# Optimization experiments

Hardware: AMD Instinct MI355X
Metric: run time of the kernel (lower is better)

Reference implementation:

```python
import jax, jax.numpy as jnp
import numpy as np

N_NODES = 100000
N_EDGES = 1600000
IN_F = 16
OUT_F = 64
PERIODS = 12
N_PHASE = 4


def setup_inputs() -> dict:
    key = jax.random.key(0)
    ks = jax.random.split(key, 12)
    inp = {
        'x': jax.random.normal(ks[0], (N_NODES, IN_F, PERIODS), jnp.float32),
        'edge_index': jax.random.randint(ks[1], (2, N_EDGES), 0, N_NODES, jnp.int64),
        'attn': jax.random.normal(ks[2], (PERIODS,), jnp.float32),
        'conv_z_w': jax.random.normal(ks[3], (IN_F, OUT_F), jnp.float32) * 0.1,
        'conv_z_b': jnp.zeros((OUT_F,), jnp.float32),
        'conv_r_w': jax.random.normal(ks[4], (IN_F, OUT_F), jnp.float32) * 0.1,
        'conv_r_b': jnp.zeros((OUT_F,), jnp.float32),
        'conv_h_w': jax.random.normal(ks[5], (IN_F, OUT_F), jnp.float32) * 0.1,
        'conv_h_b': jnp.zeros((OUT_F,), jnp.float32),
        'lin_z_w': jax.random.normal(ks[6], (2 * OUT_F, OUT_F), jnp.float32) * 0.1,
        'lin_z_b': jnp.zeros((OUT_F,), jnp.float32),
        'lin_r_w': jax.random.normal(ks[7], (2 * OUT_F, OUT_F), jnp.float32) * 0.1,
        'lin_r_b': jnp.zeros((OUT_F,), jnp.float32),
        'lin_h_w': jax.random.normal(ks[8], (2 * OUT_F, OUT_F), jnp.float32) * 0.1,
        'lin_h_b': jnp.zeros((OUT_F,), jnp.float32),
        'out_w': jax.random.normal(ks[9], (OUT_F, N_PHASE), jnp.float32) * 0.1,
        'out_b': jnp.zeros((N_PHASE,), jnp.float32),
    }
    return inp


def _gcn_norm(edge_index, num_nodes, dtype):
    # add self loops (fill value 1), symmetric normalization as in PyG gcn_norm
    loops = jnp.arange(num_nodes, dtype=edge_index.dtype)
    src = jnp.concatenate([edge_index[0], loops])
    dst = jnp.concatenate([edge_index[1], loops])
    deg = jax.ops.segment_sum(jnp.ones_like(dst, dtype=dtype), dst, num_segments=num_nodes)
    dinv = jnp.where(deg > 0, jax.lax.rsqrt(deg), jnp.zeros_like(deg))
    norm = dinv[src] * dinv[dst]  # [E + N]
    return src, dst, norm


def reference(x, edge_index, attn, conv_z_w, conv_z_b, conv_r_w, conv_r_b,
              conv_h_w, conv_h_b, lin_z_w, lin_z_b, lin_r_w, lin_r_b,
              lin_h_w, lin_h_b, out_w, out_b):
    N = x.shape[0]
    periods = x.shape[2]
    F_out = conv_z_w.shape[1]
    src, dst, norm = _gcn_norm(edge_index, N, x.dtype)

    def conv(Xp, W, b):
        XW = Xp @ W                                   # [N, F_out]
        msg = norm[:, None] * XW[src]                 # gather over edges
        return jax.ops.segment_sum(msg, dst, num_segments=N) + b

    probs = jax.nn.softmax(attn)
    H0 = jnp.zeros((N, F_out), x.dtype)  # A3TGCN never carries H between periods
    H_accum = jnp.zeros((N, F_out), x.dtype)
    for p in range(periods):
        Xp = x[:, :, p]
        Z = jax.nn.sigmoid(jnp.concatenate([conv(Xp, conv_z_w, conv_z_b), H0], axis=1) @ lin_z_w + lin_z_b)
        R = jax.nn.sigmoid(jnp.concatenate([conv(Xp, conv_r_w, conv_r_b), H0], axis=1) @ lin_r_w + lin_r_b)
        Ht = jnp.tanh(jnp.concatenate([conv(Xp, conv_h_w, conv_h_b), H0 * R], axis=1) @ lin_h_w + lin_h_b)
        H = Z * H0 + (1.0 - Z) * Ht
        H_accum = H_accum + probs[p] * H

    h = jax.nn.relu(H_accum)
    logits = h @ out_w + out_b
    return jax.nn.softmax(logits, axis=1)
```

## Files before the change

### kernel.cpp

```cpp
#include <hip/hip_runtime.h>
#include <math.h>

#define NN 100000
#define NE 1600000
#define PERIODS 12
#define SLOTS 48
#define NBUCK 391
#define FRAG 256
#define CAPB 48
#define PTH 512

typedef unsigned short ushort_t;
typedef __attribute__((ext_vector_type(8))) short short8;
typedef __attribute__((ext_vector_type(16))) float floatx16;
typedef __attribute__((ext_vector_type(2))) float f32x2;

union F4S8 { float4 f; short8 s; int4 i; };

__device__ __forceinline__ ushort_t f2bf(float f) {
  unsigned u = __float_as_uint(f);
  unsigned r = u + 0x7fffu + ((u >> 16) & 1u);
  return (ushort_t)(r >> 16);
}

__device__ __forceinline__ f32x2 unpk(unsigned u) {
  f32x2 t;
  t.x = __uint_as_float(u << 16);
  t.y = __uint_as_float(u & 0xffff0000u);
  return t;
}
__device__ __forceinline__ void pkadd(f32x2& a, f32x2 t) {
  asm("v_pk_add_f32 %0, %0, %1" : "+v"(a) : "v"(t));
}

__global__ __launch_bounds__(PTH) void k_part(
    const int* __restrict__ src, const int* __restrict__ dst,
    int* __restrict__ cnt_blk, int* __restrict__ part,
    const float* __restrict__ attn,
    const float* __restrict__ czw, const float* __restrict__ czb,
    const float* __restrict__ chw, const float* __restrict__ chb,
    const float* __restrict__ lzw, const float* __restrict__ lzb,
    const float* __restrict__ lhw, const float* __restrict__ lhb,
    ushort_t* __restrict__ Bz32, ushort_t* __restrict__ Bh32,
    float2* __restrict__ cb2, float* __restrict__ probs_ext) {
  if (blockIdx.x == FRAG) {
    for (int t5 = threadIdx.x; t5 < 1024; t5 += PTH) {
      int f = t5 >> 6, c = t5 & 63;
      float az = 0.f, ah = 0.f;
#pragma unroll 8
      for (int k = 0; k < 64; ++k) {
        az += czw[f * 64 + k] * lzw[k * 64 + c];
        ah += chw[f * 64 + k] * lhw[k * 64 + c];
      }
      int idx = (((c >> 5) * 64) + ((f >> 3) * 32) + (c & 31)) * 8 + (f & 7);
      Bz32[idx] = f2bf(az);
      Bh32[idx] = f2bf(ah);
    }
    if (threadIdx.x < 64) {
      int t = threadIdx.x;
      float vz = lzb[t], vh = lhb[t];
      for (int k = 0; k < 64; ++k) {
        vz += czb[k] * lzw[k * 64 + t];
        vh += chb[k] * lhw[k * 64 + t];
      }
      cb2[t] = make_float2(vz, vh);
    }
    if (threadIdx.x == 0) {
      float m = -1e30f;
      for (int p = 0; p < PERIODS; ++p) m = fmaxf(m, attn[p]);
      float e[PERIODS], s = 0.f;
      for (int p = 0; p < PERIODS; ++p) { e[p] = __expf(attn[p] - m); s += e[p]; }
      float inv = 1.f / s;
      for (int r = 0; r < 32; ++r)
        probs_ext[r] = (r < 12) ? e[r] * inv : ((r < 24) ? e[r - 12] * inv : 0.f);
    }
    return;
  }
  __shared__ int cnt[NBUCK];
  int tid = threadIdx.x, blk = blockIdx.x;
  for (int c = tid; c < NBUCK; c += PTH) cnt[c] = 0;
  __syncthreads();
  for (unsigned i = blk * (unsigned)PTH + tid; i < NE / 4; i += FRAG * (unsigned)PTH) {
    int4 dv = ((const int4*)dst)[i];
    int4 sv = ((const int4*)src)[i];
    int d[4] = {dv.x, dv.y, dv.z, dv.w};
    int s[4] = {sv.x, sv.y, sv.z, sv.w};
#pragma unroll
    for (int k = 0; k < 4; ++k) {
      int cls = d[k] >> 8;
      int slot = atomicAdd(&cnt[cls], 1);
      if (slot < CAPB)
        part[(size_t)(cls * FRAG + blk) * CAPB + slot] = (d[k] & 255) | (s[k] << 8);
    }
  }
  __syncthreads();
  for (int c = tid; c < NBUCK; c += PTH) cnt_blk[blk * NBUCK + c] = cnt[c];
}

__global__ __launch_bounds__(512) void k_csr(const int* __restrict__ cnt_blk,
                                             const int* __restrict__ part,
                                             int* __restrict__ deg,
                                             int* __restrict__ csr) {
  __shared__ int cnt[256];
  int b = blockIdx.x, tid = threadIdx.x;
  if (tid < 256) cnt[tid] = 0;
  __syncthreads();
  int f = tid & 255, sub = tid >> 8;
  int c = cnt_blk[f * NBUCK + b];
  c = c < CAPB ? c : CAPB;
  const int* cell = part + (size_t)(b * FRAG + f) * CAPB;
  for (int i = sub; i < c; i += 2) {
    int r = cell[i];
    int dl = r & 255;
    int slot = atomicAdd(&cnt[dl], 1);
    if (slot < SLOTS)
      csr[((size_t)(b * 256 + dl)) * SLOTS + slot] = (r >> 8) * 384;
  }
  __syncthreads();
  int node = b * 256 + tid;
  if (tid < 256 && node < NN) {
    int cc = cnt[tid];
    deg[node] = cc;
    int cl = cc < SLOTS ? cc : SLOTS;
    int padded = (cl + 3) & ~3;
    int* row = csr + (size_t)node * SLOTS;
    for (int sl = cl; sl < padded; ++sl) row[sl] = NN * 384;
  }
}

__global__ __launch_bounds__(256) void k_prescale(const float* __restrict__ x,
                                                  const int* __restrict__ deg,
                                                  ushort_t* __restrict__ xs) {
  __shared__ float st[4][192];
  int wid = threadIdx.x >> 6, l = threadIdx.x & 63;
  int n = blockIdx.x * 4 + wid;
  if (n > NN || l >= 48) return;
  char* ob = (char*)xs;
  if (n == NN) {
    uint2 z; z.x = 0u; z.y = 0u;
    *(uint2*)(ob + (size_t)NN * 384 + l * 8) = z;
    return;
  }
  float4 v4 = *(const float4*)(x + (size_t)n * 192 + 4 * l);
  *(float4*)&st[wid][4 * l] = v4;
  asm volatile("s_waitcnt lgkmcnt(0)" ::: "memory");
  float dn = rsqrtf((float)(deg[n] + 1));
  float v[4];
#pragma unroll
  for (int c = 0; c < 4; ++c) {
    int o = 4 * l + c;
    v[c] = dn * st[wid][(o & 15) * 12 + (o >> 4)];
  }
  uint2 w;
  w.x = (unsigned)f2bf(v[0]) | ((unsigned)f2bf(v[1]) << 16);
  w.y = (unsigned)f2bf(v[2]) | ((unsigned)f2bf(v[3]) << 16);
  *(uint2*)(ob + (size_t)n * 384 + l * 8) = w;
}

__global__ __launch_bounds__(256) void k_main(
    const ushort_t* __restrict__ xs, const int* __restrict__ csr,
    const int* __restrict__ deg,
    const ushort_t* __restrict__ Bz32, const ushort_t* __restrict__ Bh32,
    const float2* __restrict__ cb2, const float* __restrict__ probs_ext,
    const float* __restrict__ out_w, const float* __restrict__ out_b,
    float* __restrict__ out) {
  __shared__ ushort_t Alds[4][32][16];
  int wid = __builtin_amdgcn_readfirstlane(threadIdx.x >> 6);
  int l = threadIdx.x & 63;
  int nA = blockIdx.x * 8 + wid * 2;
  int nB = nA + 1;
  char* albase = (char*)&Alds[wid][0][0];
  if (l < 16) *(int4*)(albase + 768 + l * 16) = make_int4(0, 0, 0, 0);

  const char* xb = (const char*)xs;
  unsigned loff = (unsigned)(l < 48 ? l : 47) * 8u;

  int2 dd = *(const int2*)(deg + nA);
  int dA = dd.x, dB = dd.y;
  int cA = dA < SLOTS ? dA : SLOTS, cB = dB < SLOTS ? dB : SLOTS;
  int KA = (cA + 3) >> 2, KB = (cB + 3) >> 2;
  const int* bktA = csr + (size_t)nA * SLOTS;
  const int* bktB = bktA + SLOTS;

  uint2 sA = *(const uint2*)(xb + (unsigned)nA * 384u + loff);
  uint2 sB = *(const uint2*)(xb + (unsigned)nB * 384u + loff);
  f32x2 aA01 = unpk(sA.x), aA23 = unpk(sA.y);
  f32x2 aB01 = unpk(sB.x), aB23 = unpk(sB.y);

  uint2 qa[4], qb[4];
  auto issue4 = [&](const int* bkt, int k, uint2* q) {
    int4 e = ((const int4*)bkt)[k];
    q[0] = *(const uint2*)(xb + (unsigned)e.x + loff);
    q[1] = *(const uint2*)(xb + (unsigned)e.y + loff);
    q[2] = *(const uint2*)(xb + (unsigned)e.z + loff);
    q[3] = *(const uint2*)(xb + (unsigned)e.w + loff);
  };
  auto accA4 = [&](const uint2* q) {
#pragma unroll
    for (int j = 0; j < 4; ++j) { pkadd(aA01, unpk(q[j].x)); pkadd(aA23, unpk(q[j].y)); }
  };
  auto accB4 = [&](const uint2* q) {
#pragma unroll
    for (int j = 0; j < 4; ++j) { pkadd(aB01, unpk(q[j].x)); pkadd(aB23, unpk(q[j].y)); }
  };

  int km = KA < KB ? KA : KB;
  int k = 0;
  for (; k < km; ++k) {
    issue4(bktA, k, qa);
    issue4(bktB, k, qb);
    accA4(qa);
    accB4(qb);
  }
  for (; k < KA; ++k) { issue4(bktA, k, qa); accA4(qa); }
  for (; k < KB; ++k) { issue4(bktB, k, qb); accB4(qb); }

  float dnA = rsqrtf((float)(dA + 1)), dnB = rsqrtf((float)(dB + 1));

  if (l < 48) {
    uint2 wA, wB;
    wA.x = (unsigned)f2bf(dnA * aA01.x) | ((unsigned)f2bf(dnA * aA01.y) << 16);
    wA.y = (unsigned)f2bf(dnA * aA23.x) | ((unsigned)f2bf(dnA * aA23.y) << 16);
    wB.x = (unsigned)f2bf(dnB * aB01.x) | ((unsigned)f2bf(dnB * aB01.y) << 16);
    wB.y = (unsigned)f2bf(dnB * aB23.x) | ((unsigned)f2bf(dnB * aB23.y) << 16);
    *(uint2*)(albase + l * 8) = wA;
    *(uint2*)(albase + 384 + l * 8) = wB;
  }
  asm volatile("s_waitcnt lgkmcnt(0)" ::: "memory");
  F4S8 afr;
  afr.f = *(const float4*)(albase + (unsigned)(l & 31) * 32u + (unsigned)(l >> 5) * 16u);

  float2 cbv0 = cb2[l & 31], cbv1 = cb2[(l & 31) + 32];
  float prv[12];
  unsigned sby = (l & 32u) >> 1;
#pragma unroll
  for (int r = 0; r < 12; ++r) {
    const int rb = (r & 3) + 8 * (r >> 2);
    prv[r] = *(const float*)((const char*)probs_ext + rb * 4 + sby);
  }
  bool sh = (l & 32) != 0;
  float hA[2], hB[2];

  floatx16 zero16;
#pragma unroll
  for (int r = 0; r < 16; ++r) zero16[r] = 0.f;

  auto gates = [&](const floatx16& az, const floatx16& ah, float2 cbv, int t) {
    float g0 = 0.f, g1 = 0.f, g2 = 0.f;
#pragma unroll
    for (int r = 0; r < 12; ++r) {
      float zz = az[r] + cbv.x;
      float hh = ah[r] + cbv.y;
      float ez = __expf(zz);
      float e2h = __expf(2.f * hh);
      float val = (e2h - 1.f) * __builtin_amdgcn_rcpf((1.f + ez) * (e2h + 1.f));
      float c = prv[r] * val;
      if ((r >> 2) == 0) g0 += c;
      else if ((r >> 2) == 1) g1 += c;
      else g2 += c;
    }
    float pa = g0 + (sh ? 0.f : g1);
    float pb = g2 + (sh ? g1 : 0.f);
    pa += __shfl_xor(pa, 32, 64);
    pb += __shfl_xor(pb, 32, 64);
    hA[t] = fmaxf(pa, 0.f);
    hB[t] = fmaxf(pb, 0.f);
  };

  {
    F4S8 bz, bh;
    bz.f = ((const float4*)Bz32)[l];
    bh.f = ((const float4*)Bh32)[l];
    floatx16 az = __builtin_amdgcn_mfma_f32_32x32x16_bf16(afr.s, bz.s, zero16, 0, 0, 0);
    floatx16 ah = __builtin_amdgcn_mfma_f32_32x32x16_bf16(afr.s, bh.s, zero16, 0, 0, 0);
    gates(az, ah, cbv0, 0);
  }
  __builtin_amdgcn_sched_barrier(0);
  {
    F4S8 bz, bh;
    bz.f = ((const float4*)Bz32)[64 + l];
    bh.f = ((const float4*)Bh32)[64 + l];
    floatx16 az = __builtin_amdgcn_mfma_f32_32x32x16_bf16(afr.s, bz.s, zero16, 0, 0, 0);
    floatx16 ah = __builtin_amdgcn_mfma_f32_32x32x16_bf16(afr.s, bh.s, zero16, 0, 0, 0);
    gates(az, ah, cbv1, 1);
  }

  int c0 = l & 31;
  float4 w0 = ((const float4*)out_w)[c0];
  float4 w1 = ((const float4*)out_w)[c0 + 32];
  float h0 = sh ? hB[0] : hA[0];
  float h1 = sh ? hB[1] : hA[1];
  float l0 = h0 * w0.x; l0 = fmaf(h1, w1.x, l0);
  float l1 = h0 * w0.y; l1 = fmaf(h1, w1.y, l1);
  float l2 = h0 * w0.z; l2 = fmaf(h1, w1.z, l2);
  float l3 = h0 * w0.w; l3 = fmaf(h1, w1.w, l3);
#pragma unroll
  for (int o = 1; o < 32; o <<= 1) {
    l0 += __shfl_xor(l0, o, 64);
    l1 += __shfl_xor(l1, o, 64);
    l2 += __shfl_xor(l2, o, 64);
    l3 += __shfl_xor(l3, o, 64);
  }
  l0 += out_b[0]; l1 += out_b[1]; l2 += out_b[2]; l3 += out_b[3];
  float m = fmaxf(fmaxf(l0, l1), fmaxf(l2, l3));
  float e0 = __expf(l0 - m), e1 = __expf(l1 - m), e2 = __expf(l2 - m), e3 = __expf(l3 - m);
  float inv = __builtin_amdgcn_rcpf(e0 + e1 + e2 + e3);
  if (c0 < 4) {
    float v = (c0 == 0) ? e0 * inv : (c0 == 1) ? e1 * inv : (c0 == 2) ? e2 * inv : e3 * inv;
    out[(size_t)(sh ? nB : nA) * 4 + c0] = v;
  }
}

extern "C" void kernel_launch(void* const* d_in, const int* in_sizes, int n_in,
                              void* d_out, int out_size, void* d_ws, size_t ws_size,
                              hipStream_t stream) {
  const float* x    = (const float*)d_in[0];
  const int*   ei   = (const int*)d_in[1];
  const float* attn = (const float*)d_in[2];
  const float* czw  = (const float*)d_in[3];
  const float* czb  = (const float*)d_in[4];
  const float* chw  = (const float*)d_in[7];
  const float* chb  = (const float*)d_in[8];
  const float* lzw  = (const float*)d_in[9];
  const float* lzb  = (const float*)d_in[10];
  const float* lhw  = (const float*)d_in[13];
  const float* lhb  = (const float*)d_in[14];
  const float* outw = (const float*)d_in[15];
  const float* outb = (const float*)d_in[16];
  float* out = (float*)d_out;

  char* ws = (char*)d_ws;
  size_t off = 0;
  auto alloc = [&](size_t bytes) {
    void* p = ws + off;
    off += (bytes + 255) & ~(size_t)255;
    return p;
  };
  int*      deg       = (int*)alloc((size_t)NN * 4);
  int*      csr       = (int*)alloc((size_t)NN * SLOTS * 4);
  void*     shared_region = alloc((size_t)(NN + 1) * 384);
  int*      part      = (int*)shared_region;
  ushort_t* xs        = (ushort_t*)shared_region;
  int*      cnt_blk   = (int*)alloc((size_t)FRAG * NBUCK * 4);
  ushort_t* Bz32      = (ushort_t*)alloc(2 * 64 * 8 * 2);
  ushort_t* Bh32      = (ushort_t*)alloc(2 * 64 * 8 * 2);
  float2*   cb2       = (float2*)alloc(64 * 8);
  float*    probs_ext = (float*)alloc(32 * 4);

  k_part<<<FRAG + 1, PTH, 0, stream>>>(ei, ei + NE, cnt_blk, part,
                                       attn, czw, czb, chw, chb,
                                       lzw, lzb, lhw, lhb,
                                       Bz32, Bh32, cb2, probs_ext);
  k_csr<<<NBUCK, 512, 0, stream>>>(cnt_blk, part, deg, csr);
  k_prescale<<<NN / 4 + 1, 256, 0, stream>>>(x, deg, xs);
  k_main<<<NN / 8, 256, 0, stream>>>(xs, csr, deg, Bz32, Bh32, cb2, probs_ext,
                                     outw, outb, out);
}
```

Before: 289.1 us.

## Fuse partition, CSR build and prescale into one cooperative kernel

```diff
diff --git a/kernel.cpp b/kernel.cpp
--- a/kernel.cpp
+++ b/kernel.cpp
@@ -1,5 +1,8 @@
 #include <hip/hip_runtime.h>
+#include <hip/hip_cooperative_groups.h>
 #include <math.h>
+
+namespace cg = cooperative_groups;
 
 #define NN 100000
 #define NE 1600000
@@ -8,7 +11,7 @@
 #define NBUCK 391
 #define FRAG 256
 #define CAPB 48
-#define PTH 512
+#define CGRID 1024
 
 typedef unsigned short ushort_t;
 typedef __attribute__((ext_vector_type(8))) short short8;
@@ -33,7 +36,7 @@
   asm("v_pk_add_f32 %0, %0, %1" : "+v"(a) : "v"(t));
 }
 
-__global__ __launch_bounds__(PTH) void k_part(
+__global__ __launch_bounds__(256) void k_prep(
     const int* __restrict__ src, const int* __restrict__ dst,
     int* __restrict__ cnt_blk, int* __restrict__ part,
     const float* __restrict__ attn,
@@ -42,9 +45,17 @@
     const float* __restrict__ lzw, const float* __restrict__ lzb,
     const float* __restrict__ lhw, const float* __restrict__ lhb,
     ushort_t* __restrict__ Bz32, ushort_t* __restrict__ Bh32,
-    float2* __restrict__ cb2, float* __restrict__ probs_ext) {
-  if (blockIdx.x == FRAG) {
-    for (int t5 = threadIdx.x; t5 < 1024; t5 += PTH) {
+    float2* __restrict__ cb2, float* __restrict__ probs_ext,
+    int* __restrict__ deg, int* __restrict__ csr,
+    const float* __restrict__ x, ushort_t* __restrict__ xs) {
+  cg::grid_group grid = cg::this_grid();
+  __shared__ int cntp[NBUCK];
+  __shared__ int cnt2[256];
+  __shared__ float st[4][192];
+  int blk = blockIdx.x, tid = threadIdx.x;
+
+  if (blk == CGRID - 1) {
+    for (int t5 = tid; t5 < 1024; t5 += 256) {
       int f = t5 >> 6, c = t5 & 63;
       float az = 0.f, ah = 0.f;
 #pragma unroll 8
@@ -56,8 +67,8 @@
       Bz32[idx] = f2bf(az);
       Bh32[idx] = f2bf(ah);
     }
-    if (threadIdx.x < 64) {
-      int t = threadIdx.x;
+    if (tid < 64) {
+      int t = tid;
       float vz = lzb[t], vh = lhb[t];
       for (int k = 0; k < 64; ++k) {
         vz += czb[k] * lzw[k * 64 + t];
@@ -65,7 +76,7 @@
       }
       cb2[t] = make_float2(vz, vh);
     }
-    if (threadIdx.x == 0) {
+    if (tid == 0) {
       float m = -1e30f;
       for (int p = 0; p < PERIODS; ++p) m = fmaxf(m, attn[p]);
       float e[PERIODS], s = 0.f;
@@ -74,87 +85,88 @@
       for (int r = 0; r < 32; ++r)
         probs_ext[r] = (r < 12) ? e[r] * inv : ((r < 24) ? e[r - 12] * inv : 0.f);
     }
-    return;
-  }
-  __shared__ int cnt[NBUCK];
-  int tid = threadIdx.x, blk = blockIdx.x;
-  for (int c = tid; c < NBUCK; c += PTH) cnt[c] = 0;
-  __syncthreads();
-  for (unsigned i = blk * (unsigned)PTH + tid; i < NE / 4; i += FRAG * (unsigned)PTH) {
-    int4 dv = ((const int4*)dst)[i];
-    int4 sv = ((const int4*)src)[i];
-    int d[4] = {dv.x, dv.y, dv.z, dv.w};
-    int s[4] = {sv.x, sv.y, sv.z, sv.w};
-#pragma unroll
-    for (int k = 0; k < 4; ++k) {
-      int cls = d[k] >> 8;
-      int slot = atomicAdd(&cnt[cls], 1);
-      if (slot < CAPB)
-        part[(size_t)(cls * FRAG + blk) * CAPB + slot] = (d[k] & 255) | (s[k] << 8);
-    }
-  }
-  __syncthreads();
-  for (int c = tid; c < NBUCK; c += PTH) cnt_blk[blk * NBUCK + c] = cnt[c];
-}
-
-__global__ __launch_bounds__(512) void k_csr(const int* __restrict__ cnt_blk,
-                                             const int* __restrict__ part,
-                                             int* __restrict__ deg,
-                                             int* __restrict__ csr) {
-  __shared__ int cnt[256];
-  int b = blockIdx.x, tid = threadIdx.x;
-  if (tid < 256) cnt[tid] = 0;
-  __syncthreads();
-  int f = tid & 255, sub = tid >> 8;
-  int c = cnt_blk[f * NBUCK + b];
-  c = c < CAPB ? c : CAPB;
-  const int* cell = part + (size_t)(b * FRAG + f) * CAPB;
-  for (int i = sub; i < c; i += 2) {
-    int r = cell[i];
-    int dl = r & 255;
-    int slot = atomicAdd(&cnt[dl], 1);
-    if (slot < SLOTS)
-      csr[((size_t)(b * 256 + dl)) * SLOTS + slot] = (r >> 8) * 384;
-  }
-  __syncthreads();
-  int node = b * 256 + tid;
-  if (tid < 256 && node < NN) {
-    int cc = cnt[tid];
-    deg[node] = cc;
-    int cl = cc < SLOTS ? cc : SLOTS;
-    int padded = (cl + 3) & ~3;
-    int* row = csr + (size_t)node * SLOTS;
-    for (int sl = cl; sl < padded; ++sl) row[sl] = NN * 384;
-  }
-}
-
-__global__ __launch_bounds__(256) void k_prescale(const float* __restrict__ x,
-                                                  const int* __restrict__ deg,
-                                                  ushort_t* __restrict__ xs) {
-  __shared__ float st[4][192];
-  int wid = threadIdx.x >> 6, l = threadIdx.x & 63;
-  int n = blockIdx.x * 4 + wid;
-  if (n > NN || l >= 48) return;
-  char* ob = (char*)xs;
-  if (n == NN) {
-    uint2 z; z.x = 0u; z.y = 0u;
-    *(uint2*)(ob + (size_t)NN * 384 + l * 8) = z;
-    return;
-  }
-  float4 v4 = *(const float4*)(x + (size_t)n * 192 + 4 * l);
-  *(float4*)&st[wid][4 * l] = v4;
-  asm volatile("s_waitcnt lgkmcnt(0)" ::: "memory");
-  float dn = rsqrtf((float)(deg[n] + 1));
-  float v[4];
-#pragma unroll
-  for (int c = 0; c < 4; ++c) {
-    int o = 4 * l + c;
-    v[c] = dn * st[wid][(o & 15) * 12 + (o >> 4)];
-  }
-  uint2 w;
-  w.x = (unsigned)f2bf(v[0]) | ((unsigned)f2bf(v[1]) << 16);
-  w.y = (unsigned)f2bf(v[2]) | ((unsigned)f2bf(v[3]) << 16);
-  *(uint2*)(ob + (size_t)n * 384 + l * 8) = w;
+  } else if (blk < FRAG) {
+    for (int c = tid; c < NBUCK; c += 256) cntp[c] = 0;
+    __syncthreads();
+    for (unsigned i = blk * 256u + tid; i < NE / 4; i += FRAG * 256u) {
+      int4 dv = ((const int4*)dst)[i];
+      int4 sv = ((const int4*)src)[i];
+      int d[4] = {dv.x, dv.y, dv.z, dv.w};
+      int s[4] = {sv.x, sv.y, sv.z, sv.w};
+#pragma unroll
+      for (int k = 0; k < 4; ++k) {
+        int cls = d[k] >> 8;
+        int slot = atomicAdd(&cntp[cls], 1);
+        if (slot < CAPB)
+          part[(size_t)(cls * FRAG + blk) * CAPB + slot] = (d[k] & 255) | (s[k] << 8);
+      }
+    }
+    __syncthreads();
+    for (int c = tid; c < NBUCK; c += 256) cnt_blk[blk * NBUCK + c] = cntp[c];
+  }
+  grid.sync();
+
+  if (blk < NBUCK) {
+    cnt2[tid] = 0;
+    __syncthreads();
+    int b = blk, f = tid;
+    int c = cnt_blk[f * NBUCK + b];
+    c = c < CAPB ? c : CAPB;
+    const int* cell = part + (size_t)(b * FRAG + f) * CAPB;
+    for (int i = 0; i < c; i += 4) {
+      int4 r4 = *(const int4*)(cell + i);
+      int rr[4] = {r4.x, r4.y, r4.z, r4.w};
+#pragma unroll
+      for (int j = 0; j < 4; ++j) {
+        if (i + j < c) {
+          int r = rr[j];
+          int dl = r & 255;
+          int slot = atomicAdd(&cnt2[dl], 1);
+          if (slot < SLOTS)
+            csr[((size_t)(b * 256 + dl)) * SLOTS + slot] = (r >> 8) * 384;
+        }
+      }
+    }
+    __syncthreads();
+    int node = b * 256 + tid;
+    if (node < NN) {
+      int cc = cnt2[tid];
+      deg[node] = cc;
+      int cl = cc < SLOTS ? cc : SLOTS;
+      int padded = (cl + 3) & ~3;
+      int* row = csr + (size_t)node * SLOTS;
+      for (int sl = cl; sl < padded; ++sl) row[sl] = NN * 384;
+    }
+  }
+  grid.sync();
+
+  {
+    int wid = tid >> 6, l = tid & 63;
+    char* ob = (char*)xs;
+    for (int g = blk; g <= NN / 4; g += CGRID) {
+      int n = g * 4 + wid;
+      if (n > NN || l >= 48) continue;
+      if (n == NN) {
+        uint2 z; z.x = 0u; z.y = 0u;
+        *(uint2*)(ob + (size_t)NN * 384 + l * 8) = z;
+        continue;
+      }
+      float4 v4 = *(const float4*)(x + (size_t)n * 192 + 4 * l);
+      *(float4*)&st[wid][4 * l] = v4;
+      asm volatile("s_waitcnt lgkmcnt(0)" ::: "memory");
+      float dn = rsqrtf((float)(deg[n] + 1));
+      float v[4];
+#pragma unroll
+      for (int c = 0; c < 4; ++c) {
+        int o = 4 * l + c;
+        v[c] = dn * st[wid][(o & 15) * 12 + (o >> 4)];
+      }
+      uint2 w;
+      w.x = (unsigned)f2bf(v[0]) | ((unsigned)f2bf(v[1]) << 16);
+      w.y = (unsigned)f2bf(v[2]) | ((unsigned)f2bf(v[3]) << 16);
+      *(uint2*)(ob + (size_t)n * 384 + l * 8) = w;
+    }
+  }
 }
 
 __global__ __launch_bounds__(256) void k_main(
@@ -347,12 +359,17 @@
   float2*   cb2       = (float2*)alloc(64 * 8);
   float*    probs_ext = (float*)alloc(32 * 4);
 
-  k_part<<<FRAG + 1, PTH, 0, stream>>>(ei, ei + NE, cnt_blk, part,
-                                       attn, czw, czb, chw, chb,
-                                       lzw, lzb, lhw, lhb,
-                                       Bz32, Bh32, cb2, probs_ext);
-  k_csr<<<NBUCK, 512, 0, stream>>>(cnt_blk, part, deg, csr);
-  k_prescale<<<NN / 4 + 1, 256, 0, stream>>>(x, deg, xs);
+  const int* srcp = ei;
+  const int* dstp = ei + NE;
+  void* kargs[] = {
+    (void*)&srcp, (void*)&dstp, (void*)&cnt_blk, (void*)&part,
+    (void*)&attn, (void*)&czw, (void*)&czb, (void*)&chw, (void*)&chb,
+    (void*)&lzw, (void*)&lzb, (void*)&lhw, (void*)&lhb,
+    (void*)&Bz32, (void*)&Bh32, (void*)&cb2, (void*)&probs_ext,
+    (void*)&deg, (void*)&csr, (void*)&x, (void*)&xs
+  };
+  hipLaunchCooperativeKernel((const void*)k_prep, dim3(CGRID), dim3(256),
+                             kargs, 0, stream);
   k_main<<<NN / 8, 256, 0, stream>>>(xs, csr, deg, Bz32, Bh32, cb2, probs_ext,
                                      outw, outb, out);
 }
```

Measured after the change: 576.1 us. +99.3%, slower.
